# Optimization experiments

Hardware: AMD Instinct MI355X
Metric: run time of the kernel (lower is better)

## Reference

```python
import jax, jax.numpy as jnp
import numpy as np

# MACE TensorProductConv with in_irreps=128x0e, sh_irreps=0e+1o+2e+3o,
# every CG path 0e (x) l -> l is the identity, so the fused tensor product is
# out[e, c, (l, m)] = w[e, l, c] * x_src[e, c] * sh[e, (l, m)].
# SymmetricContraction is a stub (pass) in the given source, treated as identity.

N_SRC = 10000
N_DST = 10000
E = 100000
C = 128           # channel multiplicity
LS = (0, 1, 2, 3) # spherical-harmonic degrees; dims 1,3,5,7 -> sh dim 16
SH_DIM = sum(2 * l + 1 for l in LS)
MLP_IN = 64
MLP_HID = 128
W_NUMEL = len(LS) * C  # 512 tensor-product weights per edge


def setup_inputs() -> dict:
    key = jax.random.key(0)
    ks = jax.random.split(key, 7)
    return {
        "src_features": jax.random.normal(ks[0], (N_SRC, C), dtype=jnp.float32),
        "edge_sh": jax.random.normal(ks[1], (E, SH_DIM), dtype=jnp.float32),
        "edge_emb": jax.random.normal(ks[2], (E, MLP_IN), dtype=jnp.float32),
        "W1": jax.random.normal(ks[3], (MLP_IN, MLP_HID), dtype=jnp.float32),
        "W2": jax.random.normal(ks[4], (MLP_HID, W_NUMEL), dtype=jnp.float32),
        "src": jax.random.randint(ks[5], (E,), 0, N_SRC),
        "dst": jax.random.randint(ks[6], (E,), 0, N_DST),
        "num_dst_nodes": N_DST,
    }


def _mlp(edge_emb, W1, W2):
    # e3nn FullyConnectedNet: normalized linear layers, silu on hidden only.
    h = jax.nn.silu(edge_emb @ (W1 / np.sqrt(MLP_IN)))
    return h @ (W2 / np.sqrt(MLP_HID))  # [E, W_NUMEL]


def reference(src_features, edge_sh, edge_emb, W1, W2, src, dst, num_dst_nodes):
    tp_w = _mlp(edge_emb, W1, W2).reshape(-1, len(LS), C)  # [E, L, C]
    x_src = src_features[src]                                # gather: [E, C]
    outs = []
    off = 0
    for i, l in enumerate(LS):
        d = 2 * l + 1
        sh_l = edge_sh[:, off:off + d]                       # [E, d]
        # weighted scalar-times-SH tensor product: [E, C, d]
        o = (tp_w[:, i, :] * x_src)[:, :, None] * sh_l[:, None, :]
        outs.append(o.reshape(o.shape[0], C * d))
        off += d
    out_e = jnp.concatenate(outs, axis=-1)                   # [E, 2048]
    # scatter-reduce sum onto destination nodes
    node_out = jax.ops.segment_sum(out_e, dst, num_segments=num_dst_nodes)
    # SymmetricContraction stub -> identity
    return node_out
```

## Files before the change

### kernel.cpp

```cpp
#include <hip/hip_runtime.h>
#include <math.h>

#define C_DIM 128
#define SHD   16
#define HID   128
#define MIN_D 64
#define OUT_PER_NODE 2048
#define BLK   256
#define MBLK  512
#define SCAN_T 1024
#define MT    128

#define HST 136

typedef __attribute__((ext_vector_type(8))) short bf16x8;
typedef __attribute__((ext_vector_type(4))) float f32x4;

__device__ __forceinline__ unsigned f2bf_u(float x) {
    unsigned u = __builtin_bit_cast(unsigned, x);
    return (u + 0x7fffu + ((u >> 16) & 1u)) >> 16;
}
__device__ __forceinline__ short f2bf(float x) { return (short)f2bf_u(x); }
__device__ __forceinline__ unsigned packbf2(float a, float b) {
    return f2bf_u(a) | (f2bf_u(b) << 16);
}
__device__ __forceinline__ float bf2f(unsigned h) {
    return __builtin_bit_cast(float, h << 16);
}

__global__ void prep_kernel(const int* __restrict__ dst, int* counts, int E,
                            const float* __restrict__ W1, const float* __restrict__ W2,
                            short* __restrict__ w1t, short* __restrict__ w2t,
                            int HB) {
    int b = blockIdx.x;
    int t = threadIdx.x;
    if (b < HB) {
        int i = b * BLK + t;
        if (i < E) atomicAdd(&counts[dst[i]], 1);
    } else {
        int i = (b - HB) * BLK + t;
        if (i < MIN_D * HID) {
            int n = i >> 6, k = i & 63;
            w1t[i] = f2bf(W1[k * HID + n] * 0.125f);
        } else if (i < MIN_D * HID + HID * 512) {
            int j = i - MIN_D * HID;
            int p = j >> 7, ks = j & 127;
            int nt = p >> 4, m16 = p & 15;
            int jcol = 64 * (nt >> 2) + 4 * m16 + (nt & 3);
            int ka   = (2 * (ks >> 5) + (ks & 1)) * 16 + ((ks >> 1) & 15);
            w2t[j] = f2bf(W2[ka * 512 + jcol] * 0.0883883476483184f);
        }
    }
}

__global__ __launch_bounds__(SCAN_T)
void scan_kernel(const int* __restrict__ counts, int* row_ptr, int* cursor, int n) {
    const int t = threadIdx.x;
    const int per = (n + SCAN_T - 1) / SCAN_T;
    int lp[16];
    int base = t * per;
    int sum = 0;
    for (int i = 0; i < per && i < 16; ++i) {
        int idx = base + i;
        int v = (idx < n) ? counts[idx] : 0;
        lp[i] = sum;
        sum += v;
    }
    __shared__ int sbuf[SCAN_T];
    sbuf[t] = sum;
    __syncthreads();
    for (int off = 1; off < SCAN_T; off <<= 1) {
        int v = (t >= off) ? sbuf[t - off] : 0;
        __syncthreads();
        sbuf[t] += v;
        __syncthreads();
    }
    int excl = (t == 0) ? 0 : sbuf[t - 1];
    for (int i = 0; i < per && i < 16; ++i) {
        int idx = base + i;
        if (idx < n) {
            int rp = excl + lp[i];
            row_ptr[idx] = rp;
            cursor[idx]  = rp;
        }
    }
    if (t == SCAN_T - 1) row_ptr[n] = sbuf[SCAN_T - 1];
}

__global__ void scatter_kernel(const int* __restrict__ dst, const int* __restrict__ src,
                               int* cursor, int2* es_list, int E) {
    int i = blockIdx.x * blockDim.x + threadIdx.x;
    if (i < E) {
        int pos = atomicAdd(&cursor[dst[i]], 1);
        es_list[pos] = make_int2(i, src[i]);
    }
}

__global__ __launch_bounds__(MBLK)
void mlp_kernel(const float* __restrict__ edge_emb,
                const short* __restrict__ w1t,
                const short* __restrict__ w2t,
                unsigned* __restrict__ tp_u,
                int E)
{
    const int t    = threadIdx.x;
    const int lane = t & 63;
    const int w    = t >> 6;
    const int m16  = lane & 15;
    const int q    = lane >> 4;
    const int e0   = blockIdx.x * MT;

    __shared__ __align__(16) short hb[MT * HST];
    unsigned* hb_u = (unsigned*)hb;

    union CVT { unsigned u[4]; bf16x8 v; };

    bf16x8 a[2];
    {
        const int row = e0 + w * 16 + m16;
        if (row < E) {
            const float* rp = &edge_emb[(size_t)row * MIN_D];
#pragma unroll
            for (int ks = 0; ks < 2; ++ks) {
                float4 v0 = *(const float4*)&rp[ks * 32 + q * 8];
                float4 v1 = *(const float4*)&rp[ks * 32 + q * 8 + 4];
                CVT c;
                c.u[0] = packbf2(v0.x, v0.y);
                c.u[1] = packbf2(v0.z, v0.w);
                c.u[2] = packbf2(v1.x, v1.y);
                c.u[3] = packbf2(v1.z, v1.w);
                a[ks] = c.v;
            }
        } else {
            CVT c; c.u[0] = c.u[1] = c.u[2] = c.u[3] = 0u;
            a[0] = c.v; a[1] = c.v;
        }
    }

#pragma unroll
    for (int u2 = 0; u2 < 4; ++u2) {
        f32x4 c0 = {0.f, 0.f, 0.f, 0.f}, c1 = {0.f, 0.f, 0.f, 0.f};
#pragma unroll
        for (int ks = 0; ks < 2; ++ks) {
            bf16x8 b0 = *(const bf16x8*)&w1t[((2 * u2) * 16 + m16) * MIN_D + ks * 32 + q * 8];
            bf16x8 b1 = *(const bf16x8*)&w1t[((2 * u2 + 1) * 16 + m16) * MIN_D + ks * 32 + q * 8];
            c0 = __builtin_amdgcn_mfma_f32_16x16x32_bf16(a[ks], b0, c0, 0, 0, 0);
            c1 = __builtin_amdgcn_mfma_f32_16x16x32_bf16(a[ks], b1, c1, 0, 0, 0);
        }
#pragma unroll
        for (int r = 0; r < 4; ++r) {
            int hrow = w * 16 + q * 4 + r;
            float z0 = c0[r], z1 = c1[r];
            float h0 = z0 / (1.f + __expf(-z0));
            float h1 = z1 / (1.f + __expf(-z1));
            hb_u[hrow * (HST / 2) + 16 * u2 + m16] = packbf2(h0, h1);
        }
    }

    bf16x8 B[4][4];
#pragma unroll
    for (int j = 0; j < 4; ++j)
#pragma unroll
        for (int ks = 0; ks < 4; ++ks)
            B[j][ks] = *(const bf16x8*)&w2t[((4 * w + j) * 16 + m16) * HID + ks * 32 + q * 8];

    __syncthreads();

    const int d0 = 32 * w + 2 * m16;
    for (int mt = 0; mt < 8; ++mt) {
        bf16x8 av[4];
#pragma unroll
        for (int ks = 0; ks < 4; ++ks)
            av[ks] = *(const bf16x8*)&hb[(mt * 16 + m16) * HST + ks * 32 + q * 8];
        f32x4 acc[4];
#pragma unroll
        for (int j = 0; j < 4; ++j) acc[j] = (f32x4){0.f, 0.f, 0.f, 0.f};
#pragma unroll
        for (int ks = 0; ks < 4; ++ks)
#pragma unroll
            for (int j = 0; j < 4; ++j)
                acc[j] = __builtin_amdgcn_mfma_f32_16x16x32_bf16(av[ks], B[j][ks], acc[j], 0, 0, 0);
#pragma unroll
        for (int r = 0; r < 4; ++r) {
            int e = e0 + mt * 16 + q * 4 + r;
            if (e < E) {
                uint2 u;
                u.x = packbf2(acc[0][r], acc[1][r]);
                u.y = packbf2(acc[2][r], acc[3][r]);
                *(uint2*)&tp_u[(size_t)e * 256 + d0] = u;
            }
        }
    }
}

template<int L>
__device__ __forceinline__ void tp_node(
    const float* __restrict__ src_features,
    const float* __restrict__ edge_sh,
    const unsigned* __restrict__ tp_u,
    const int2* __restrict__ es_list,
    float* __restrict__ out,
    int n, int t, int rbeg, int rend)
{
    constexpr int D = 2 * L + 1;
    constexpr int SHOFF = L * L;
    const int c0 = (2 * t) & 127;
    const int obase = 128 * L * L + c0 * D;

    float accA[D], accB[D];
#pragma unroll
    for (int m = 0; m < D; ++m) { accA[m] = 0.f; accB[m] = 0.f; }

    for (int i = rbeg; i < rend; i += 8) {
        int2 es[8];
#pragma unroll
        for (int k = 0; k < 8; ++k) {
            int idx = i + k;
            int vi  = (idx < rend) ? idx : (rend - 1);
            es[k] = es_list[vi];
        }
        unsigned tp2[8]; float2 x[8]; float sh[8][D];
#pragma unroll
        for (int k = 0; k < 8; ++k) {
            unsigned v = tp_u[(size_t)es[k].x * 256 + t];
            tp2[k] = (i + k < rend) ? v : 0u;
            x[k]   = *(const float2*)&src_features[(size_t)es[k].y * C_DIM + c0];
            const float* shp = &edge_sh[(size_t)es[k].x * SHD + SHOFF];
#pragma unroll
            for (int m = 0; m < D; ++m) sh[k][m] = shp[m];
        }
#pragma unroll
        for (int k = 0; k < 8; ++k) {
            float wx0 = bf2f(tp2[k] & 0xffffu) * x[k].x;
            float wx1 = bf2f(tp2[k] >> 16)     * x[k].y;
#pragma unroll
            for (int m = 0; m < D; ++m) {
                accA[m] += wx0 * sh[k][m];
                accB[m] += wx1 * sh[k][m];
            }
        }
    }

    float* op = out + (size_t)n * OUT_PER_NODE + obase;
#pragma unroll
    for (int m = 0; m < D; ++m) op[m] = accA[m];
#pragma unroll
    for (int m = 0; m < D; ++m) op[D + m] = accB[m];
}

__global__ __launch_bounds__(BLK)
void tp_kernel(const float* __restrict__ src_features,
               const float* __restrict__ edge_sh,
               const unsigned* __restrict__ tp_u,
               const int* __restrict__ row_ptr,
               const int2* __restrict__ es_list,
               float* __restrict__ out)
{
    const int n = blockIdx.x;
    const int t = threadIdx.x;
    const int l = t >> 6;
    const int rbeg = row_ptr[n];
    const int rend = row_ptr[n + 1];
    if (l == 0)      tp_node<0>(src_features, edge_sh, tp_u, es_list, out, n, t, rbeg, rend);
    else if (l == 1) tp_node<1>(src_features, edge_sh, tp_u, es_list, out, n, t, rbeg, rend);
    else if (l == 2) tp_node<2>(src_features, edge_sh, tp_u, es_list, out, n, t, rbeg, rend);
    else             tp_node<3>(src_features, edge_sh, tp_u, es_list, out, n, t, rbeg, rend);
}


extern "C" void kernel_launch(void* const* d_in, const int* in_sizes, int n_in,
                              void* d_out, int out_size, void* d_ws, size_t ws_size,
                              hipStream_t stream) {
    const float* src_features = (const float*)d_in[0];
    const float* edge_sh      = (const float*)d_in[1];
    const float* edge_emb     = (const float*)d_in[2];
    const float* W1           = (const float*)d_in[3];
    const float* W2           = (const float*)d_in[4];
    const int*   src          = (const int*)d_in[5];
    const int*   dst          = (const int*)d_in[6];

    const int E     = in_sizes[5];
    const int N_DST = out_size / OUT_PER_NODE;
    const int EB    = (E + MT - 1) / MT;

    char* p = (char*)d_ws;
    short* w1t      = (short*)p;              p += MIN_D * HID * 2;
    short* w2t      = (short*)p;              p += HID * 512 * 2;
    unsigned* tp_u  = (unsigned*)p;           p += (size_t)EB * MT * 1024;
    int2* es_list   = (int2*)p;               p += (size_t)E * 8;
    int* counts     = (int*)p;                p += 16384 * 4;
    int* row_ptr    = (int*)p;                p += 16384 * 4;
    int* cursor     = (int*)p;                p += 16384 * 4;

    const int HB = (E + BLK - 1) / BLK;
    const int CB = (MIN_D * HID + HID * 512 + BLK - 1) / BLK;

    (void)hipMemsetAsync(counts, 0, (size_t)N_DST * 4, stream);
    prep_kernel<<<HB + CB, BLK, 0, stream>>>(dst, counts, E, W1, W2, w1t, w2t, HB);
    scan_kernel<<<1, SCAN_T, 0, stream>>>(counts, row_ptr, cursor, N_DST);
    scatter_kernel<<<(E + 255) / 256, 256, 0, stream>>>(dst, src, cursor, es_list, E);
    mlp_kernel<<<EB, MBLK, 0, stream>>>(edge_emb, w1t, w2t, tp_u, E);
    tp_kernel<<<N_DST, BLK, 0, stream>>>(src_features, edge_sh, tp_u,
                                         row_ptr, es_list, (float*)d_out);
}
```

Measured before the change: 229.8 us.

## Fuse CSR build preprocessing into one cooperative kernel with grid syncs

```diff
diff --git a/kernel.cpp b/kernel.cpp
--- a/kernel.cpp
+++ b/kernel.cpp
@@ -1,5 +1,8 @@
 #include <hip/hip_runtime.h>
+#include <hip/hip_cooperative_groups.h>
 #include <math.h>
+
+namespace cg = cooperative_groups;
 
 #define C_DIM 128
 #define SHD   16
@@ -8,8 +11,8 @@
 #define OUT_PER_NODE 2048
 #define BLK   256
 #define MBLK  512
-#define SCAN_T 1024
 #define MT    128
+#define PGRID 256
 
 #define HST 136
 
@@ -28,21 +31,25 @@
     return __builtin_bit_cast(float, h << 16);
 }
 
-__global__ void prep_kernel(const int* __restrict__ dst, int* counts, int E,
-                            const float* __restrict__ W1, const float* __restrict__ W2,
-                            short* __restrict__ w1t, short* __restrict__ w2t,
-                            int HB) {
-    int b = blockIdx.x;
-    int t = threadIdx.x;
-    if (b < HB) {
-        int i = b * BLK + t;
-        if (i < E) atomicAdd(&counts[dst[i]], 1);
-    } else {
-        int i = (b - HB) * BLK + t;
+__global__ __launch_bounds__(BLK)
+void prep_coop(const int* __restrict__ dst, const int* __restrict__ src,
+               const float* __restrict__ W1, const float* __restrict__ W2,
+               short* __restrict__ w1t, short* __restrict__ w2t,
+               int* __restrict__ counts, int* __restrict__ row_ptr,
+               int* __restrict__ cursor, int* __restrict__ bsum,
+               int2* __restrict__ es_list, int E, int n_dst)
+{
+    cg::grid_group grid = cg::this_grid();
+    const int tx = threadIdx.x;
+    const int g  = blockIdx.x * BLK + tx;
+    const int GS = gridDim.x * BLK;
+
+    for (int i = g; i < n_dst; i += GS) counts[i] = 0;
+    for (int i = g; i < MIN_D * HID + HID * 512; i += GS) {
         if (i < MIN_D * HID) {
             int n = i >> 6, k = i & 63;
             w1t[i] = f2bf(W1[k * HID + n] * 0.125f);
-        } else if (i < MIN_D * HID + HID * 512) {
+        } else {
             int j = i - MIN_D * HID;
             int p = j >> 7, ks = j & 127;
             int nt = p >> 4, m16 = p & 15;
@@ -51,46 +58,47 @@
             w2t[j] = f2bf(W2[ka * 512 + jcol] * 0.0883883476483184f);
         }
     }
-}
-
-__global__ __launch_bounds__(SCAN_T)
-void scan_kernel(const int* __restrict__ counts, int* row_ptr, int* cursor, int n) {
-    const int t = threadIdx.x;
-    const int per = (n + SCAN_T - 1) / SCAN_T;
-    int lp[16];
-    int base = t * per;
-    int sum = 0;
-    for (int i = 0; i < per && i < 16; ++i) {
-        int idx = base + i;
-        int v = (idx < n) ? counts[idx] : 0;
-        lp[i] = sum;
-        sum += v;
-    }
-    __shared__ int sbuf[SCAN_T];
-    sbuf[t] = sum;
+    grid.sync();
+
+    for (int i = g; i < E; i += GS) atomicAdd(&counts[dst[i]], 1);
+    grid.sync();
+
+    __shared__ int sb[BLK];
+    int v = (g < n_dst) ? counts[g] : 0;
+    sb[tx] = v;
     __syncthreads();
-    for (int off = 1; off < SCAN_T; off <<= 1) {
-        int v = (t >= off) ? sbuf[t - off] : 0;
+    for (int off = 1; off < BLK; off <<= 1) {
+        int x = (tx >= off) ? sb[tx - off] : 0;
         __syncthreads();
-        sbuf[t] += v;
+        sb[tx] += x;
         __syncthreads();
     }
-    int excl = (t == 0) ? 0 : sbuf[t - 1];
-    for (int i = 0; i < per && i < 16; ++i) {
-        int idx = base + i;
-        if (idx < n) {
-            int rp = excl + lp[i];
-            row_ptr[idx] = rp;
-            cursor[idx]  = rp;
-        }
-    }
-    if (t == SCAN_T - 1) row_ptr[n] = sbuf[SCAN_T - 1];
-}
-
-__global__ void scatter_kernel(const int* __restrict__ dst, const int* __restrict__ src,
-                               int* cursor, int2* es_list, int E) {
-    int i = blockIdx.x * blockDim.x + threadIdx.x;
-    if (i < E) {
+    int incl = sb[tx];
+    if (tx == BLK - 1) bsum[blockIdx.x] = incl;
+    grid.sync();
+
+    if (blockIdx.x == 0) {
+        int bv = bsum[tx];
+        __syncthreads();
+        sb[tx] = bv;
+        __syncthreads();
+        for (int off = 1; off < BLK; off <<= 1) {
+            int x = (tx >= off) ? sb[tx - off] : 0;
+            __syncthreads();
+            sb[tx] += x;
+            __syncthreads();
+        }
+        bsum[tx] = sb[tx];
+    }
+    grid.sync();
+
+    int boff = (blockIdx.x == 0) ? 0 : bsum[blockIdx.x - 1];
+    int excl = boff + incl - v;
+    if (g < n_dst) { row_ptr[g] = excl; cursor[g] = excl; }
+    if (g == n_dst - 1) row_ptr[n_dst] = excl + v;
+    grid.sync();
+
+    for (int i = g; i < E; i += GS) {
         int pos = atomicAdd(&cursor[dst[i]], 1);
         es_list[pos] = make_int2(i, src[i]);
     }
@@ -291,14 +299,16 @@
     int* counts     = (int*)p;                p += 16384 * 4;
     int* row_ptr    = (int*)p;                p += 16384 * 4;
     int* cursor     = (int*)p;                p += 16384 * 4;
-
-    const int HB = (E + BLK - 1) / BLK;
-    const int CB = (MIN_D * HID + HID * 512 + BLK - 1) / BLK;
-
-    (void)hipMemsetAsync(counts, 0, (size_t)N_DST * 4, stream);
-    prep_kernel<<<HB + CB, BLK, 0, stream>>>(dst, counts, E, W1, W2, w1t, w2t, HB);
-    scan_kernel<<<1, SCAN_T, 0, stream>>>(counts, row_ptr, cursor, N_DST);
-    scatter_kernel<<<(E + 255) / 256, 256, 0, stream>>>(dst, src, cursor, es_list, E);
+    int* bsum       = (int*)p;                p += PGRID * 4;
+
+    void* cargs[] = {
+        (void*)&dst, (void*)&src, (void*)&W1, (void*)&W2,
+        (void*)&w1t, (void*)&w2t, (void*)&counts, (void*)&row_ptr,
+        (void*)&cursor, (void*)&bsum, (void*)&es_list,
+        (void*)&E, (void*)&N_DST
+    };
+    (void)hipLaunchCooperativeKernel((void*)prep_coop, dim3(PGRID), dim3(BLK),
+                                     cargs, 0, stream);
     mlp_kernel<<<EB, MBLK, 0, stream>>>(edge_emb, w1t, w2t, tp_u, E);
     tp_kernel<<<N_DST, BLK, 0, stream>>>(src_features, edge_sh, tp_u,
                                          row_ptr, es_list, (float*)d_out);
```

After: 363.5 us. +58.2%, slower.
